# Optimization experiments

Hardware: AMD Instinct MI355X
Metric: run time of the kernel (lower is better)

Reference implementation:

```python
import jax, jax.numpy as jnp
import numpy as np

N = 4096          # batch size
D = 1024          # embedding dim
NUM_INSTANCES = 8 # samples per class (balanced batch, required by the original resize logic)
ALPHA = 20.0
MARGIN = 0.5


def setup_inputs() -> dict:
    key = jax.random.key(0)
    inputs = jax.random.normal(key, (N, D), dtype=jnp.float32)
    # balanced targets: each class appears exactly NUM_INSTANCES times
    targets = (jnp.arange(N, dtype=jnp.int32) // NUM_INSTANCES).astype(jnp.int32)
    return {"inputs": inputs, "targets": targets}


def reference(inputs, targets):
    n = inputs.shape[0]
    k_pos = NUM_INSTANCES - 1          # positives per row (excl. self)
    k_neg = n - NUM_INSTANCES          # negatives per row

    # L2 normalize rows, cosine similarity matrix [n, n]
    x = inputs / jnp.linalg.norm(inputs, axis=1, keepdims=True)
    sim = x @ x.T

    same = targets[:, None] == targets[None, :]
    eye = jnp.eye(n, dtype=bool)
    pos_mask = same & ~eye             # positives, diag removed
    neg_mask = ~same                   # negatives

    INF = jnp.float32(1e9)
    # per-row sorted positive / negative sims (ascending); fixed-size slices
    pos_sorted = jnp.sort(jnp.where(pos_mask, sim, INF), axis=1)[:, :k_pos]   # [n, k_pos]
    neg_sorted = jnp.sort(jnp.where(neg_mask, sim, INF), axis=1)[:, :k_neg]   # [n, k_neg]

    # base = max(max(sim) - 0.1, margin + 0.2)
    base = jnp.maximum(jnp.max(sim) - 0.1, MARGIN + 0.2)

    # dynamic selection expressed as masks over fixed-size sorted arrays
    neg_keep = neg_sorted > (pos_sorted[:, :1] - 0.05)   # negatives above min positive - 0.05
    pos_keep = pos_sorted < base                          # positives below base

    pos_elem = jnp.log1p(jnp.exp(-2.0 * (pos_sorted - MARGIN)))   # [n, k_pos]
    neg_elem = jnp.log1p(jnp.exp(ALPHA * (neg_sorted - MARGIN)))  # [n, k_neg]

    pos_cnt = pos_keep.sum(axis=1)
    neg_cnt = neg_keep.sum(axis=1)

    pos_mean = (pos_elem * pos_keep).sum(axis=1) / jnp.maximum(pos_cnt, 1).astype(sim.dtype)
    neg_mean = (neg_elem * neg_keep).sum(axis=1) / jnp.maximum(neg_cnt, 1).astype(sim.dtype)

    # fallbacks: empty pos set -> smallest positive; empty neg set -> largest negative
    pos_loss = jnp.where(pos_cnt > 0, pos_mean, pos_elem[:, 0])
    neg_loss = jnp.where(neg_cnt > 0, neg_mean, neg_elem[:, -1])

    return jnp.mean(pos_loss + neg_loss)   # sum over rows / n
```

## Files before the change

kernel.cpp:

```cpp
#include <hip/hip_runtime.h>
#include <hip/hip_bf16.h>
#include <hip/hip_fp8.h>
#include <math.h>

#define N 4096
#define D 1024
#define NINST 8
#define NGROUP (N / NINST)
#define ALPHA 20.0f
#define MARGIN 0.5f
#define NB2 32
#define NTILE2 (NB2 * (NB2 + 1) / 2)

typedef __attribute__((ext_vector_type(4))) float f32x4;

__device__ __forceinline__ unsigned fkey(float f) {
    int b = __float_as_int(f);
    return (b >= 0) ? ((unsigned)b | 0x80000000u) : ~(unsigned)b;
}
__device__ __forceinline__ float fdec(unsigned u) {
    int b = (u & 0x80000000u) ? (int)(u ^ 0x80000000u) : ~(int)u;
    return __int_as_float(b);
}

__device__ __forceinline__ float softplus(float x) {
    float z = __expf(-fabsf(x));
    return fmaxf(x, 0.0f) + __logf(1.0f + z);
}

__device__ __forceinline__ void gld16(const void* g, void* l) {
    __builtin_amdgcn_global_load_lds(
        (const __attribute__((address_space(1))) void*)g,
        (__attribute__((address_space(3))) void*)l, 16, 0, 0);
}

__global__ __launch_bounds__(512) void k_normpos(const float* __restrict__ in,
                                                 unsigned long* __restrict__ xn8,
                                                 float* __restrict__ pos_sims,
                                                 float* __restrict__ min_pos,
                                                 unsigned* __restrict__ gmax,
                                                 float* __restrict__ accum,
                                                 unsigned* __restrict__ cnt) {
    __shared__ float4 srows4[8 * 257];
    __shared__ float spart[8][4];
    __shared__ float sinv[8];
    __shared__ float sg[8][8];

    int g = blockIdx.x;
    int t = threadIdx.x;
    int lane = t & 63;
    int w = t >> 6;
    int par = t >> 8;

    if (g == 0) {
        if (t == 0) { *gmax = 0u; *cnt = 0u; }
        if (t < 32) accum[t] = 0.f;
    }

    const float4* in4 = (const float4*)in;
    #pragma unroll
    for (int k = 0; k < 4; ++k) {
        float4 v = in4[(size_t)g * 2048 + k * 512 + t];
        int row = 2 * k + par;
        srows4[row * 257 + (t & 255)] = v;
        float ss = v.x * v.x + v.y * v.y + v.z * v.z + v.w * v.w;
        #pragma unroll
        for (int off = 1; off < 64; off <<= 1) ss += __shfl_xor(ss, off);
        if (lane == 0) spart[row][w & 3] = ss;
    }
    __syncthreads();
    if (t < 8) sinv[t] = rsqrtf(spart[t][0] + spart[t][1] + spart[t][2] + spart[t][3]);
    __syncthreads();

    {
        int i_row = t & 7;
        int oct  = (t >> 3) & 3;
        int k0b  = (t >> 5) & 7;
        int hi   = t >> 8;
        size_t base = (size_t)(g >> 3) * 8192 + (size_t)((g >> 1) & 3) * 64
                    + (size_t)(oct * 16 + (g & 1) * 8 + i_row);
        float inv = sinv[i_row];
        #pragma unroll
        for (int jj = 0; jj < 2; ++jj) {
            int k0 = k0b + (hi * 2 + jj) * 8;
            float4 v0 = srows4[i_row * 257 + k0 * 8 + oct * 2];
            float4 v1 = srows4[i_row * 257 + k0 * 8 + oct * 2 + 1];
            union { unsigned char c[8]; unsigned long u64; } o;
            o.c[0] = __hip_fp8_e4m3(v0.x * inv).__x;
            o.c[1] = __hip_fp8_e4m3(v0.y * inv).__x;
            o.c[2] = __hip_fp8_e4m3(v0.z * inv).__x;
            o.c[3] = __hip_fp8_e4m3(v0.w * inv).__x;
            o.c[4] = __hip_fp8_e4m3(v1.x * inv).__x;
            o.c[5] = __hip_fp8_e4m3(v1.y * inv).__x;
            o.c[6] = __hip_fp8_e4m3(v1.z * inv).__x;
            o.c[7] = __hip_fp8_e4m3(v1.w * inv).__x;
            xn8[base + (size_t)k0 * 256] = o.u64;
        }
    }

    int pair = t >> 3, a = pair >> 3, b = pair & 7, slice = t & 7;
    const float4* pa = srows4 + a * 257 + slice * 32;
    const float4* pb = srows4 + b * 257 + slice * 32;
    int j0 = ((pair << 1) + slice) & 31;
    float s = 0.f;
    #pragma unroll 8
    for (int i = 0; i < 32; ++i) {
        int j = (i + j0) & 31;
        float4 x = pa[j], y = pb[j];
        s += x.x * y.x + x.y * y.y + x.z * y.z + x.w * y.w;
    }
    s += __shfl_xor(s, 1);
    s += __shfl_xor(s, 2);
    s += __shfl_xor(s, 4);
    if (slice == 0) sg[a][b] = s * sinv[a] * sinv[b];
    __syncthreads();
    if (t < 8) {
        float mn = 1e30f;
        int idx = 0;
        #pragma unroll
        for (int b2 = 0; b2 < 8; ++b2) {
            if (b2 == t) continue;
            float v = sg[t][b2];
            mn = fminf(mn, v);
            pos_sims[(size_t)(g * 8 + t) * 8 + idx] = v;
            ++idx;
        }
        min_pos[g * 8 + t] = mn;
    }
}

__global__ __launch_bounds__(256, 4) void k_neg(const unsigned long* __restrict__ xn8,
                                                const float* __restrict__ min_pos,
                                                float* __restrict__ sum_part,
                                                int* __restrict__ cnt_part,
                                                float* __restrict__ max_part,
                                                unsigned* __restrict__ gmax) {
    __shared__ char sbuf[2][8192];
    __shared__ float sMinA[128];
    __shared__ float sMinB[128];

    int bid = blockIdx.x;
    int rt = 0, rem = bid;
    while (rem >= NB2 - rt) { rem -= NB2 - rt; ++rt; }
    int ct = rt + rem;
    bool diag = (rt == ct);

    int R0 = rt * 128, C0 = ct * 128;
    int t = threadIdx.x, l = t & 63, w = t >> 6;
    int wr = w >> 1, wc = w & 1;
    int lrow = l & 15;
    int kgrp = l >> 4;

    if (t < 128) { sMinA[t] = min_pos[R0 + t]; sMinB[t] = min_pos[C0 + t]; }

    int half = w & 1;
    int isB = w >> 1;
    int pbase = diag ? R0 : (isB ? C0 : R0);
    const char* gsrc = (const char*)xn8 + (size_t)((pbase >> 6) + half) * 65536 + (size_t)l * 16;
    unsigned ldso = (unsigned)(isB * 4096 + half * 2048);

    #define STAGE(buf, s_)                                              \
        do {                                                            \
            char* d_ = sbuf[buf] + ldso;                                \
            gld16(gsrc + (size_t)(s_) * 2048,        d_);               \
            gld16(gsrc + (size_t)(s_) * 2048 + 1024, d_ + 1024);        \
        } while (0)

    f32x4 zero = {0.f, 0.f, 0.f, 0.f};
    f32x4 acc[4][4];
    #pragma unroll
    for (int m = 0; m < 4; ++m)
        #pragma unroll
        for (int n = 0; n < 4; ++n) acc[m][n] = zero;

    STAGE(0, 0);
    __syncthreads();

    for (int it = 0; it < 32; ++it) {
        if (it + 1 < 32) STAGE((it & 1) ^ 1, it + 1);

        const char* bufp = sbuf[it & 1];
        const char* fA = bufp + wr * 2048 + l * 8;
        const char* fB = bufp + 4096 + wc * 2048 + l * 8;
        long a[4], b[4];
        #pragma unroll
        for (int m = 0; m < 4; ++m) {
            a[m] = *(const long*)(fA + m * 512);
            b[m] = *(const long*)(fB + m * 512);
        }
        #pragma unroll
        for (int m = 0; m < 4; ++m)
            #pragma unroll
            for (int n = 0; n < 4; ++n)
                acc[m][n] = __builtin_amdgcn_mfma_f32_16x16x32_fp8_fp8(
                    a[m], b[n], acc[m][n], 0, 0, 0);

        __syncthreads();
    }
    #undef STAGE

    float allmax = -1e30f;
    int cbase = C0 + wc * 64;
    int pcRow = ct * 2 + wc;
    int pcCol = rt * 2 + wr;

    float thB[4];
    #pragma unroll
    for (int n = 0; n < 4; ++n) thB[n] = sMinB[wc * 64 + n * 16 + lrow] - 0.05f;

    float colS[4] = {0.f, 0.f, 0.f, 0.f};
    float colM[4] = {-1e30f, -1e30f, -1e30f, -1e30f};
    int   colC[4] = {0, 0, 0, 0};

    #pragma unroll
    for (int m = 0; m < 4; ++m) {
        #pragma unroll
        for (int reg = 0; reg < 4; ++reg) {
            int lr = wr * 64 + m * 16 + kgrp * 4 + reg;
            int grow = R0 + lr;
            float th = sMinA[lr] - 0.05f;
            int gi = grow >> 3;
            float rs = 0.f, rm = -1e30f;
            int rc = 0;
            #pragma unroll
            for (int n = 0; n < 4; ++n) {
                int gcol = cbase + n * 16 + lrow;
                float s = acc[m][n][reg];
                allmax = fmaxf(allmax, s);
                if ((gcol >> 3) != gi) {
                    float e = softplus(ALPHA * (s - MARGIN));
                    rm = fmaxf(rm, s);
                    if (s > th) { rs += e; rc += 1; }
                    if (!diag) {
                        colM[n] = fmaxf(colM[n], s);
                        if (s > thB[n]) { colS[n] += e; colC[n] += 1; }
                    }
                }
            }
            #pragma unroll
            for (int off = 1; off < 16; off <<= 1) {
                rs += __shfl_xor(rs, off);
                rc += __shfl_xor(rc, off);
                rm = fmaxf(rm, __shfl_xor(rm, off));
            }
            if (lrow == 0) {
                sum_part[(size_t)grow * 64 + pcRow] = rs;
                cnt_part[(size_t)grow * 64 + pcRow] = rc;
                max_part[(size_t)grow * 64 + pcRow] = rm;
            }
        }
    }

    if (!diag) {
        #pragma unroll
        for (int n = 0; n < 4; ++n) {
            float cs = colS[n], cm = colM[n];
            int cc = colC[n];
            cs += __shfl_xor(cs, 16); cs += __shfl_xor(cs, 32);
            cc += __shfl_xor(cc, 16); cc += __shfl_xor(cc, 32);
            cm = fmaxf(cm, __shfl_xor(cm, 16));
            cm = fmaxf(cm, __shfl_xor(cm, 32));
            if (kgrp == 0) {
                int gcol = cbase + n * 16 + lrow;
                sum_part[(size_t)gcol * 64 + pcCol] = cs;
                cnt_part[(size_t)gcol * 64 + pcCol] = cc;
                max_part[(size_t)gcol * 64 + pcCol] = cm;
            }
        }
    }

    #pragma unroll
    for (int off = 1; off < 64; off <<= 1) allmax = fmaxf(allmax, __shfl_xor(allmax, off));
    if (l == 0) atomicMax(gmax, fkey(allmax));
}

__global__ __launch_bounds__(256) void k_rowfinal(const float* __restrict__ sum_part,
                                                  const int* __restrict__ cnt_part,
                                                  const float* __restrict__ max_part,
                                                  const float* __restrict__ pos_sims,
                                                  const float* __restrict__ min_pos,
                                                  const unsigned* __restrict__ gmax,
                                                  float* __restrict__ accum,
                                                  unsigned* __restrict__ cnt,
                                                  float* __restrict__ out) {
    __shared__ float sloss[4];
    int row = blockIdx.x * 4 + (threadIdx.x >> 6);
    int lane = threadIdx.x & 63;
    float ns = sum_part[(size_t)row * 64 + lane];
    int nc = cnt_part[(size_t)row * 64 + lane];
    float nm = max_part[(size_t)row * 64 + lane];
    #pragma unroll
    for (int off = 1; off < 64; off <<= 1) {
        ns += __shfl_xor(ns, off);
        nc += __shfl_xor(nc, off);
        nm = fmaxf(nm, __shfl_xor(nm, off));
    }
    if (lane == 0) {
        float base = fmaxf(fdec(*gmax) - 0.1f, MARGIN + 0.2f);
        float neg_loss = (nc > 0) ? ns / (float)nc : softplus(ALPHA * (nm - MARGIN));
        float ps = 0.f;
        int pcnt = 0;
        float mn = min_pos[row];
        #pragma unroll
        for (int i = 0; i < NINST - 1; ++i) {
            float s = pos_sims[(size_t)row * 8 + i];
            if (s < base) { ps += softplus(-2.0f * (s - MARGIN)); pcnt++; }
        }
        float pos_loss = (pcnt > 0) ? ps / (float)pcnt : softplus(-2.0f * (mn - MARGIN));
        sloss[threadIdx.x >> 6] = pos_loss + neg_loss;
    }
    __syncthreads();
    if (threadIdx.x == 0) {
        float bs = sloss[0] + sloss[1] + sloss[2] + sloss[3];
        atomicAdd(&accum[blockIdx.x & 31], bs);
        __threadfence();
        unsigned old = atomicAdd(cnt, 1u);
        if (old == gridDim.x - 1) {
            __threadfence();
            float tot = 0.f;
            for (int j = 0; j < 32; ++j) tot += atomicAdd(&accum[j], 0.0f);
            out[0] = tot / (float)N;
        }
    }
}

extern "C" void kernel_launch(void* const* d_in, const int* in_sizes, int n_in,
                              void* d_out, int out_size, void* d_ws, size_t ws_size,
                              hipStream_t stream) {
    const float* in = (const float*)d_in[0];
    float* out = (float*)d_out;

    char* ws = (char*)d_ws;
    unsigned long* xn8 = (unsigned long*)(ws);
    float*   min_pos  = (float*)(ws + 8388608 + 16384);
    float*   pos_sims = (float*)(ws + 8388608 + 32768);
    float*   sum_part = (float*)(ws + 8388608 + 32768 + 131072);
    float*   max_part = (float*)(ws + 8388608 + 32768 + 131072 + 1048576);
    int*     cnt_part = (int*)  (ws + 8388608 + 32768 + 131072 + 2097152);
    unsigned* gmax    = (unsigned*)(ws + 8388608 + 32768 + 131072 + 3145728);
    float*   accum    = (float*)(ws + 8388608 + 32768 + 131072 + 3145728 + 128);
    unsigned* cnt     = (unsigned*)(ws + 8388608 + 32768 + 131072 + 3145728 + 256);

    k_normpos<<<NGROUP, 512, 0, stream>>>(in, xn8, pos_sims, min_pos, gmax, accum, cnt);
    k_neg<<<NTILE2, 256, 0, stream>>>(xn8, min_pos, sum_part, cnt_part, max_part, gmax);
    k_rowfinal<<<N / 4, 256, 0, stream>>>(sum_part, cnt_part, max_part, pos_sims, min_pos,
                                          gmax, accum, cnt, out);
}
```

Before: 101.2 us.

## Use 64x64 tiles with full-K panels staged once in LDS

The negative-pair kernel now uses 64x64 output tiles over a 64x64 triangular grid (2080 blocks) instead of 128x128 tiles (528 blocks). Each block loads its full 64xD fp8 row and column panels into 128KB of LDS in one pass, with no per-step double buffering or barriers, then runs the MFMA loop from LDS. Per-row and per-column partial reductions are combined across warps in shared memory before a single global write. The goal is more blocks for better CU fill and fewer synchronisations. In exchange, the large LDS footprint caps occupancy at about one block per CU, the load is not overlapped with compute, and smaller tiles mean more global reloads of the input.

```diff
diff --git a/kernel.cpp b/kernel.cpp
--- a/kernel.cpp
+++ b/kernel.cpp
@@ -9,8 +9,8 @@
 #define NGROUP (N / NINST)
 #define ALPHA 20.0f
 #define MARGIN 0.5f
-#define NB2 32
-#define NTILE2 (NB2 * (NB2 + 1) / 2)
+#define NB 64
+#define NTILE (NB * (NB + 1) / 2)
 
 typedef __attribute__((ext_vector_type(4))) float f32x4;
 
@@ -129,102 +129,90 @@
     }
 }
 
-__global__ __launch_bounds__(256, 4) void k_neg(const unsigned long* __restrict__ xn8,
-                                                const float* __restrict__ min_pos,
-                                                float* __restrict__ sum_part,
-                                                int* __restrict__ cnt_part,
-                                                float* __restrict__ max_part,
-                                                unsigned* __restrict__ gmax) {
-    __shared__ char sbuf[2][8192];
-    __shared__ float sMinA[128];
-    __shared__ float sMinB[128];
+__global__ __launch_bounds__(256) void k_neg(const unsigned long* __restrict__ xn8,
+                                             const float* __restrict__ min_pos,
+                                             float* __restrict__ sum_part,
+                                             int* __restrict__ cnt_part,
+                                             float* __restrict__ max_part,
+                                             unsigned* __restrict__ gmax) {
+    __shared__ __align__(16) char panels[131072];
+    __shared__ float sMinA[64], sMinB[64];
+    __shared__ float sRS[2][64]; __shared__ int sRC[2][64]; __shared__ float sRM[2][64];
+    __shared__ float sCS[2][64]; __shared__ int sCC[2][64]; __shared__ float sCM[2][64];
 
     int bid = blockIdx.x;
     int rt = 0, rem = bid;
-    while (rem >= NB2 - rt) { rem -= NB2 - rt; ++rt; }
+    while (rem >= NB - rt) { rem -= NB - rt; ++rt; }
     int ct = rt + rem;
     bool diag = (rt == ct);
 
-    int R0 = rt * 128, C0 = ct * 128;
+    int R0 = rt * 64, C0 = ct * 64;
     int t = threadIdx.x, l = t & 63, w = t >> 6;
     int wr = w >> 1, wc = w & 1;
-    int lrow = l & 15;
-    int kgrp = l >> 4;
-
-    if (t < 128) { sMinA[t] = min_pos[R0 + t]; sMinB[t] = min_pos[C0 + t]; }
-
-    int half = w & 1;
-    int isB = w >> 1;
-    int pbase = diag ? R0 : (isB ? C0 : R0);
-    const char* gsrc = (const char*)xn8 + (size_t)((pbase >> 6) + half) * 65536 + (size_t)l * 16;
-    unsigned ldso = (unsigned)(isB * 4096 + half * 2048);
-
-    #define STAGE(buf, s_)                                              \
-        do {                                                            \
-            char* d_ = sbuf[buf] + ldso;                                \
-            gld16(gsrc + (size_t)(s_) * 2048,        d_);               \
-            gld16(gsrc + (size_t)(s_) * 2048 + 1024, d_ + 1024);        \
-        } while (0)
+    int lrow = l & 15, kgrp = l >> 4;
+
+    if (t < 64) sMinA[t] = min_pos[R0 + t];
+    else if (t < 128) sMinB[t - 64] = min_pos[C0 + (t - 64)];
+
+    {
+        const char* xb = (const char*)xn8;
+        const char* src = (w < 2)
+            ? xb + (size_t)rt * 65536 + (size_t)w * 32768
+            : xb + (size_t)ct * 65536 + (size_t)(w - 2) * 32768;
+        char* dst = panels + (size_t)w * 32768;
+        #pragma unroll
+        for (int j = 0; j < 32; ++j)
+            gld16(src + (size_t)j * 1024 + (size_t)l * 16, dst + (size_t)j * 1024);
+    }
+    asm volatile("s_waitcnt vmcnt(0)" ::: "memory");
+    __syncthreads();
 
     f32x4 zero = {0.f, 0.f, 0.f, 0.f};
-    f32x4 acc[4][4];
-    #pragma unroll
-    for (int m = 0; m < 4; ++m)
-        #pragma unroll
-        for (int n = 0; n < 4; ++n) acc[m][n] = zero;
-
-    STAGE(0, 0);
-    __syncthreads();
-
-    for (int it = 0; it < 32; ++it) {
-        if (it + 1 < 32) STAGE((it & 1) ^ 1, it + 1);
-
-        const char* bufp = sbuf[it & 1];
-        const char* fA = bufp + wr * 2048 + l * 8;
-        const char* fB = bufp + 4096 + wc * 2048 + l * 8;
-        long a[4], b[4];
-        #pragma unroll
-        for (int m = 0; m < 4; ++m) {
-            a[m] = *(const long*)(fA + m * 512);
-            b[m] = *(const long*)(fB + m * 512);
-        }
-        #pragma unroll
-        for (int m = 0; m < 4; ++m)
-            #pragma unroll
-            for (int n = 0; n < 4; ++n)
-                acc[m][n] = __builtin_amdgcn_mfma_f32_16x16x32_fp8_fp8(
-                    a[m], b[n], acc[m][n], 0, 0, 0);
-
-        __syncthreads();
-    }
-    #undef STAGE
+    f32x4 acc[2][2];
+    #pragma unroll
+    for (int m = 0; m < 2; ++m)
+        #pragma unroll
+        for (int n = 0; n < 2; ++n) acc[m][n] = zero;
+
+    const char* pA = panels + (size_t)wr * 1024 + (size_t)l * 8;
+    const char* pB = panels + 65536 + (size_t)wc * 1024 + (size_t)l * 8;
+
+    #pragma unroll 4
+    for (int k = 0; k < 32; ++k) {
+        long a0 = *(const long*)(pA + (size_t)k * 2048);
+        long a1 = *(const long*)(pA + (size_t)k * 2048 + 512);
+        long b0 = *(const long*)(pB + (size_t)k * 2048);
+        long b1 = *(const long*)(pB + (size_t)k * 2048 + 512);
+        acc[0][0] = __builtin_amdgcn_mfma_f32_16x16x32_fp8_fp8(a0, b0, acc[0][0], 0, 0, 0);
+        acc[0][1] = __builtin_amdgcn_mfma_f32_16x16x32_fp8_fp8(a0, b1, acc[0][1], 0, 0, 0);
+        acc[1][0] = __builtin_amdgcn_mfma_f32_16x16x32_fp8_fp8(a1, b0, acc[1][0], 0, 0, 0);
+        acc[1][1] = __builtin_amdgcn_mfma_f32_16x16x32_fp8_fp8(a1, b1, acc[1][1], 0, 0, 0);
+    }
 
     float allmax = -1e30f;
-    int cbase = C0 + wc * 64;
-    int pcRow = ct * 2 + wc;
-    int pcCol = rt * 2 + wr;
-
-    float thB[4];
-    #pragma unroll
-    for (int n = 0; n < 4; ++n) thB[n] = sMinB[wc * 64 + n * 16 + lrow] - 0.05f;
-
-    float colS[4] = {0.f, 0.f, 0.f, 0.f};
-    float colM[4] = {-1e30f, -1e30f, -1e30f, -1e30f};
-    int   colC[4] = {0, 0, 0, 0};
-
-    #pragma unroll
-    for (int m = 0; m < 4; ++m) {
+
+    float thB[2];
+    #pragma unroll
+    for (int n = 0; n < 2; ++n) thB[n] = sMinB[wc * 32 + n * 16 + lrow] - 0.05f;
+
+    float colS[2] = {0.f, 0.f};
+    float colM[2] = {-1e30f, -1e30f};
+    int   colC[2] = {0, 0};
+
+    #pragma unroll
+    for (int m = 0; m < 2; ++m) {
         #pragma unroll
         for (int reg = 0; reg < 4; ++reg) {
-            int lr = wr * 64 + m * 16 + kgrp * 4 + reg;
+            int lr32 = m * 16 + kgrp * 4 + reg;
+            int lr = wr * 32 + lr32;
             int grow = R0 + lr;
             float th = sMinA[lr] - 0.05f;
             int gi = grow >> 3;
             float rs = 0.f, rm = -1e30f;
             int rc = 0;
             #pragma unroll
-            for (int n = 0; n < 4; ++n) {
-                int gcol = cbase + n * 16 + lrow;
+            for (int n = 0; n < 2; ++n) {
+                int gcol = C0 + wc * 32 + n * 16 + lrow;
                 float s = acc[m][n][reg];
                 allmax = fmaxf(allmax, s);
                 if ((gcol >> 3) != gi) {
@@ -243,17 +231,13 @@
                 rc += __shfl_xor(rc, off);
                 rm = fmaxf(rm, __shfl_xor(rm, off));
             }
-            if (lrow == 0) {
-                sum_part[(size_t)grow * 64 + pcRow] = rs;
-                cnt_part[(size_t)grow * 64 + pcRow] = rc;
-                max_part[(size_t)grow * 64 + pcRow] = rm;
-            }
+            if (lrow == 0) { sRS[wc][lr] = rs; sRC[wc][lr] = rc; sRM[wc][lr] = rm; }
         }
     }
 
     if (!diag) {
         #pragma unroll
-        for (int n = 0; n < 4; ++n) {
+        for (int n = 0; n < 2; ++n) {
             float cs = colS[n], cm = colM[n];
             int cc = colC[n];
             cs += __shfl_xor(cs, 16); cs += __shfl_xor(cs, 32);
@@ -261,12 +245,29 @@
             cm = fmaxf(cm, __shfl_xor(cm, 16));
             cm = fmaxf(cm, __shfl_xor(cm, 32));
             if (kgrp == 0) {
-                int gcol = cbase + n * 16 + lrow;
-                sum_part[(size_t)gcol * 64 + pcCol] = cs;
-                cnt_part[(size_t)gcol * 64 + pcCol] = cc;
-                max_part[(size_t)gcol * 64 + pcCol] = cm;
+                int lc = wc * 32 + n * 16 + lrow;
+                sCS[wr][lc] = cs; sCC[wr][lc] = cc; sCM[wr][lc] = cm;
             }
         }
+    }
+    __syncthreads();
+
+    if (t < 64) {
+        int r = t;
+        float rs = sRS[0][r] + sRS[1][r];
+        int   rc = sRC[0][r] + sRC[1][r];
+        float rm = fmaxf(sRM[0][r], sRM[1][r]);
+        sum_part[(size_t)(R0 + r) * 64 + ct] = rs;
+        cnt_part[(size_t)(R0 + r) * 64 + ct] = rc;
+        max_part[(size_t)(R0 + r) * 64 + ct] = rm;
+    } else if (t < 128 && !diag) {
+        int c = t - 64;
+        float cs = sCS[0][c] + sCS[1][c];
+        int   cc = sCC[0][c] + sCC[1][c];
+        float cm = fmaxf(sCM[0][c], sCM[1][c]);
+        sum_part[(size_t)(C0 + c) * 64 + rt] = cs;
+        cnt_part[(size_t)(C0 + c) * 64 + rt] = cc;
+        max_part[(size_t)(C0 + c) * 64 + rt] = cm;
     }
 
     #pragma unroll
@@ -342,7 +343,7 @@
     unsigned* cnt     = (unsigned*)(ws + 8388608 + 32768 + 131072 + 3145728 + 256);
 
     k_normpos<<<NGROUP, 512, 0, stream>>>(in, xn8, pos_sims, min_pos, gmax, accum, cnt);
-    k_neg<<<NTILE2, 256, 0, stream>>>(xn8, min_pos, sum_part, cnt_part, max_part, gmax);
+    k_neg<<<NTILE, 256, 0, stream>>>(xn8, min_pos, sum_part, cnt_part, max_part, gmax);
     k_rowfinal<<<N / 4, 256, 0, stream>>>(sum_part, cnt_part, max_part, pos_sims, min_pos,
                                           gmax, accum, cnt, out);
 }
```

After: 168.5 us. 1.67x slower.
